# Performance work log

Hardware: AMD Instinct MI355X
Metric: run time of the kernel (lower is better)

## Reference

```python
import jax, jax.numpy as jnp
import numpy as np

B, F, T, K = 131072, 1024, 100, 32  # batch, num_features, num_trees, features per tree (sqrt(F))


def setup_inputs() -> dict:
    key = jax.random.key(0)
    kx, kw = jax.random.split(key)
    x = jax.random.normal(kx, (B, F), dtype=jnp.float32)
    # per-tree random feature selection without replacement (np.random.choice replace=False)
    rng = np.random.default_rng(0)
    idx = np.argsort(rng.random((T, F)), axis=1)[:, :K].astype(np.int32)
    feature_indices = jnp.asarray(idx)
    feature_thresholds = jnp.zeros((T, K), dtype=jnp.float32)  # lazy-init zeros in original
    feature_weights = jax.random.uniform(kw, (T, K), dtype=jnp.float32)  # torch.rand
    return {
        "x": x,
        "feature_indices": feature_indices,
        "feature_thresholds": feature_thresholds,
        "feature_weights": feature_weights,
    }


def reference(x, feature_indices, feature_thresholds, feature_weights):
    # Per tree t: ws_t = sum_k (x[:, idx[t,k]] - thr[t,k]) * w[t,k]
    # Equivalent fused form: scatter weights into a dense [T, F] matrix and do one GEMM,
    # with per-tree bias sum_k thr*w. scatter-add handles any duplicate indices identically
    # to the gather-then-sum formulation.
    T_, K_ = feature_indices.shape
    tree_ids = jnp.arange(T_, dtype=feature_indices.dtype)[:, None]  # [T,1]
    W_full = jnp.zeros((T_, x.shape[1]), dtype=x.dtype).at[tree_ids, feature_indices].add(feature_weights)
    bias = jnp.sum(feature_thresholds * feature_weights, axis=1)  # [T]
    ws = x @ W_full.T - bias[None, :]  # [B, T]
    p = jax.nn.sigmoid(ws)
    pm = jnp.mean(p, axis=1)  # mean over trees; mean(1-p) = 1 - mean(p)
    return jnp.stack([1.0 - pm, pm], axis=1)  # [B, 2]
```

## Files before the change

kernel.cpp:

```cpp
#include <hip/hip_runtime.h>
#include <math.h>

constexpr int Bn = 131072;
constexpr int Fn = 1024;
constexpr int Tn = 100;
constexpr int Kn = 32;

constexpr int TP = 112;
constexpr int NF = TP / 16;
constexpr int BK = 32;
constexpr int NT = Fn / BK;
constexpr int BM = 128;
constexpr int MW = 32;
constexpr int BLOCK = 256;
constexpr int GRID = Bn / BM;

typedef __attribute__((ext_vector_type(8))) short bf16x8;
typedef __attribute__((ext_vector_type(4))) float f32x4;

using gptr_t = const __attribute__((address_space(1))) void*;
using lptr_t = __attribute__((address_space(3))) void*;

__device__ inline unsigned short f2bf(float f) {
    uint32_t u = __float_as_uint(f);
    return (unsigned short)((u + 0x7FFFu + ((u >> 16) & 1u)) >> 16);
}

__global__ __launch_bounds__(64)
void rf_prep(const int* __restrict__ fidx, const float* __restrict__ fthr,
             const float* __restrict__ fw,
             unsigned short* __restrict__ wt, float* __restrict__ bias)
{
    const int t    = blockIdx.x;
    const int lane = threadIdx.x;

    int4 z = make_int4(0, 0, 0, 0);
    int4* rowp = (int4*)(wt + (size_t)t * Fn);
    rowp[lane * 2 + 0] = z;
    rowp[lane * 2 + 1] = z;
    __syncthreads();

    float bsum = 0.f;
    if (t < Tn && lane < Kn) {
        const int   idx = fidx[t * Kn + lane];
        const float w   = fw[t * Kn + lane];
        const float th  = fthr[t * Kn + lane];
        wt[(size_t)t * Fn + idx] = f2bf(w);
        bsum = th * w;
    }
#pragma unroll
    for (int d = 1; d < 64; d <<= 1) bsum += __shfl_xor(bsum, d, 64);
    if (lane == 0) bias[t] = (t < Tn) ? bsum : 0.f;
}

__global__ __launch_bounds__(BLOCK)
void rf_gemm(const float* __restrict__ x,
             const unsigned short* __restrict__ wt,
             const float* __restrict__ bias,
             float* __restrict__ out)
{
    __shared__ float lds[2][BM * BK];

    const int lane = threadIdx.x & 63;
    const int wid  = threadIdx.x >> 6;
    const int rb   = blockIdx.x * BM;

    const int s_row = lane >> 3;
    const int s_c16 = (lane & 7) ^ s_row;

    const int a_rl  = lane & 15;
    const int a_xor = lane & 7;
    const int a_cb  = (lane >> 4) * 2;

    f32x4 acc[2][NF];
#pragma unroll
    for (int m = 0; m < 2; ++m)
#pragma unroll
        for (int f = 0; f < NF; ++f) acc[m][f] = (f32x4){0.f, 0.f, 0.f, 0.f};

    auto stage = [&](int t, int bsel) {
#pragma unroll
        for (int i = 0; i < 4; ++i) {
            const int win = wid * 4 + i;
            const int row = win * 8 + s_row;
            const float* src = x + (size_t)(rb + row) * Fn + t * BK + s_c16 * 4;
            float* dst = &lds[bsel][win * 256];
            __builtin_amdgcn_global_load_lds((gptr_t)src, (lptr_t)dst, 16, 0, 0);
        }
    };

    stage(0, 0);
    __syncthreads();

    for (int t = 0; t < NT; ++t) {
        const int cur = t & 1;
        if (t + 1 < NT) stage(t + 1, cur ^ 1);

        bf16x8 bfr[NF];
#pragma unroll
        for (int f = 0; f < NF; ++f) {
            const unsigned short* bp =
                wt + (size_t)(f * 16 + a_rl) * Fn + t * BK + (lane >> 4) * 8;
            bfr[f] = *(const bf16x8*)bp;
        }

        const float* buf = lds[cur];
        bf16x8 af[2];
#pragma unroll
        for (int m = 0; m < 2; ++m) {
            const int row = wid * MW + m * 16 + a_rl;
            const float* rp = buf + row * BK;
            float4 lo = *(const float4*)(rp + (((a_cb + 0) ^ a_xor) * 4));
            float4 hi = *(const float4*)(rp + (((a_cb + 1) ^ a_xor) * 4));
            bf16x8 v;
            v[0] = (short)f2bf(lo.x); v[1] = (short)f2bf(lo.y);
            v[2] = (short)f2bf(lo.z); v[3] = (short)f2bf(lo.w);
            v[4] = (short)f2bf(hi.x); v[5] = (short)f2bf(hi.y);
            v[6] = (short)f2bf(hi.z); v[7] = (short)f2bf(hi.w);
            af[m] = v;
        }

#pragma unroll
        for (int m = 0; m < 2; ++m)
#pragma unroll
            for (int f = 0; f < NF; ++f)
                acc[m][f] = __builtin_amdgcn_mfma_f32_16x16x32_bf16(
                    af[m], bfr[f], acc[m][f], 0, 0, 0);

        __syncthreads();
    }

    const int col = lane & 15;
    float psum[2][4] = {};
#pragma unroll
    for (int f = 0; f < NF; ++f) {
        const int  n     = f * 16 + col;
        const bool valid = n < Tn;
        const float bv   = bias[n];
#pragma unroll
        for (int m = 0; m < 2; ++m)
#pragma unroll
            for (int r = 0; r < 4; ++r) {
                const float ws = acc[m][f][r] - bv;
                const float p  = 1.f / (1.f + __expf(-ws));
                if (valid) psum[m][r] += p;
            }
    }
#pragma unroll
    for (int m = 0; m < 2; ++m)
#pragma unroll
        for (int r = 0; r < 4; ++r)
#pragma unroll
            for (int d = 1; d < 16; d <<= 1)
                psum[m][r] += __shfl_xor(psum[m][r], d, 64);

    const int g = lane >> 4;
#pragma unroll
    for (int m = 0; m < 2; ++m) {
        if (col < 4) {
            const int r   = col;
            const int row = rb + wid * MW + m * 16 + g * 4 + r;
            const float pm = psum[m][r] * (1.0f / Tn);
            *(float2*)(out + (size_t)row * 2) = make_float2(1.0f - pm, pm);
        }
    }
}

extern "C" void kernel_launch(void* const* d_in, const int* in_sizes, int n_in,
                              void* d_out, int out_size, void* d_ws, size_t ws_size,
                              hipStream_t stream) {
    const float* x    = (const float*)d_in[0];
    const int*   fidx = (const int*)  d_in[1];
    const float* fthr = (const float*)d_in[2];
    const float* fw   = (const float*)d_in[3];
    float*       out  = (float*)d_out;

    unsigned short* wt   = (unsigned short*)d_ws;
    float*          bias = (float*)((char*)d_ws + (size_t)TP * Fn * 2);

    rf_prep<<<TP, 64, 0, stream>>>(fidx, fthr, fw, wt, bias);
    rf_gemm<<<GRID, BLOCK, 0, stream>>>(x, wt, bias, out);
}
```

Measured before the change: 168.3 us.

## Double K-tile to 64, make LDS per-wave, and software-pipeline with manual vmcnt waits

Raises the K-tile to 64 and gives each wave its own LDS slice, so the block-wide __syncthreads is replaced by per-wave s_waitcnt vmcnt/lgkmcnt counts. The loop is unrolled by two and ping-pongs register buffers for the B fragments, prefetching the next tile's weights and staging the next x tile while MFMAs run. The goal is to remove barrier stalls and hide global-load latency. The risks are correctness of the hand-tuned vmcnt counts and higher register pressure under launch_bounds(256,2).

```diff
diff --git a/kernel.cpp b/kernel.cpp
--- a/kernel.cpp
+++ b/kernel.cpp
@@ -8,7 +8,8 @@
 
 constexpr int TP = 112;
 constexpr int NF = TP / 16;
-constexpr int BK = 32;
+constexpr int BK = 64;
+constexpr int KS = BK / 32;
 constexpr int NT = Fn / BK;
 constexpr int BM = 128;
 constexpr int MW = 32;
@@ -53,7 +54,7 @@
     if (lane == 0) bias[t] = (t < Tn) ? bsum : 0.f;
 }
 
-__global__ __launch_bounds__(BLOCK)
+__global__ __launch_bounds__(BLOCK, 2)
 void rf_gemm(const float* __restrict__ x,
              const unsigned short* __restrict__ wt,
              const float* __restrict__ bias,
@@ -65,12 +66,10 @@
     const int wid  = threadIdx.x >> 6;
     const int rb   = blockIdx.x * BM;
 
-    const int s_row = lane >> 3;
-    const int s_c16 = (lane & 7) ^ s_row;
-
-    const int a_rl  = lane & 15;
-    const int a_xor = lane & 7;
-    const int a_cb  = (lane >> 4) * 2;
+    const int s_r = lane >> 4;
+    const int s_p = lane & 15;
+    const int a_L = lane & 15;
+    const int a_g = lane >> 4;
 
     f32x4 acc[2][NF];
 #pragma unroll
@@ -80,54 +79,83 @@
 
     auto stage = [&](int t, int bsel) {
 #pragma unroll
-        for (int i = 0; i < 4; ++i) {
-            const int win = wid * 4 + i;
-            const int row = win * 8 + s_row;
-            const float* src = x + (size_t)(rb + row) * Fn + t * BK + s_c16 * 4;
-            float* dst = &lds[bsel][win * 256];
+        for (int i = 0; i < 8; ++i) {
+            const int row = i * 4 + s_r;
+            const int c   = s_p ^ (row & 15);
+            const float* src = x + (size_t)(rb + wid * MW + row) * Fn + t * BK + c * 4;
+            float* dst = &lds[bsel][wid * (MW * BK) + i * 256];
             __builtin_amdgcn_global_load_lds((gptr_t)src, (lptr_t)dst, 16, 0, 0);
         }
     };
 
+    auto loadB = [&](int t, bf16x8 (&bfr)[KS][NF]) {
+#pragma unroll
+        for (int ks = 0; ks < KS; ++ks)
+#pragma unroll
+            for (int f = 0; f < NF; ++f) {
+                const unsigned short* bp =
+                    wt + (size_t)(f * 16 + a_L) * Fn + t * BK + ks * 32 + a_g * 8;
+                bfr[ks][f] = *(const bf16x8*)bp;
+            }
+    };
+
+    auto readA = [&](int bsel, bf16x8 (&af)[KS][2]) {
+        const float* buf = &lds[bsel][wid * (MW * BK)];
+#pragma unroll
+        for (int ks = 0; ks < KS; ++ks)
+#pragma unroll
+            for (int m = 0; m < 2; ++m) {
+                const float* rp = buf + (m * 16 + a_L) * BK;
+                const int c0 = ks * 8 + a_g * 2;
+                float4 lo = *(const float4*)(rp + ((c0 ^ a_L) * 4));
+                float4 hi = *(const float4*)(rp + (((c0 + 1) ^ a_L) * 4));
+                bf16x8 v;
+                v[0] = (short)f2bf(lo.x); v[1] = (short)f2bf(lo.y);
+                v[2] = (short)f2bf(lo.z); v[3] = (short)f2bf(lo.w);
+                v[4] = (short)f2bf(hi.x); v[5] = (short)f2bf(hi.y);
+                v[6] = (short)f2bf(hi.z); v[7] = (short)f2bf(hi.w);
+                af[ks][m] = v;
+            }
+    };
+
+    auto mfma_all = [&](bf16x8 (&af)[KS][2], bf16x8 (&bfr)[KS][NF]) {
+#pragma unroll
+        for (int ks = 0; ks < KS; ++ks)
+#pragma unroll
+            for (int m = 0; m < 2; ++m)
+#pragma unroll
+                for (int f = 0; f < NF; ++f)
+                    acc[m][f] = __builtin_amdgcn_mfma_f32_16x16x32_bf16(
+                        af[ks][m], bfr[ks][f], acc[m][f], 0, 0, 0);
+    };
+
+    bf16x8 bA[KS][NF], bB[KS][NF];
+    bf16x8 af[KS][2];
+
     stage(0, 0);
-    __syncthreads();
-
-    for (int t = 0; t < NT; ++t) {
-        const int cur = t & 1;
-        if (t + 1 < NT) stage(t + 1, cur ^ 1);
-
-        bf16x8 bfr[NF];
-#pragma unroll
-        for (int f = 0; f < NF; ++f) {
-            const unsigned short* bp =
-                wt + (size_t)(f * 16 + a_rl) * Fn + t * BK + (lane >> 4) * 8;
-            bfr[f] = *(const bf16x8*)bp;
+    __builtin_amdgcn_sched_barrier(0);
+    loadB(0, bA);
+    __builtin_amdgcn_sched_barrier(0);
+    stage(1, 1);
+
+    for (int t = 0; t < NT; t += 2) {
+        loadB(t + 1, bB);
+        asm volatile("s_waitcnt vmcnt(36)" ::: "memory");
+        readA(0, af);
+        asm volatile("s_waitcnt lgkmcnt(0)" ::: "memory");
+        if (t + 2 < NT) stage(t + 2, 0);
+        mfma_all(af, bA);
+
+        if (t + 2 < NT) {
+            loadB(t + 2, bA);
+            asm volatile("s_waitcnt vmcnt(36)" ::: "memory");
+        } else {
+            asm volatile("s_waitcnt vmcnt(14)" ::: "memory");
         }
-
-        const float* buf = lds[cur];
-        bf16x8 af[2];
-#pragma unroll
-        for (int m = 0; m < 2; ++m) {
-            const int row = wid * MW + m * 16 + a_rl;
-            const float* rp = buf + row * BK;
-            float4 lo = *(const float4*)(rp + (((a_cb + 0) ^ a_xor) * 4));
-            float4 hi = *(const float4*)(rp + (((a_cb + 1) ^ a_xor) * 4));
-            bf16x8 v;
-            v[0] = (short)f2bf(lo.x); v[1] = (short)f2bf(lo.y);
-            v[2] = (short)f2bf(lo.z); v[3] = (short)f2bf(lo.w);
-            v[4] = (short)f2bf(hi.x); v[5] = (short)f2bf(hi.y);
-            v[6] = (short)f2bf(hi.z); v[7] = (short)f2bf(hi.w);
-            af[m] = v;
-        }
-
-#pragma unroll
-        for (int m = 0; m < 2; ++m)
-#pragma unroll
-            for (int f = 0; f < NF; ++f)
-                acc[m][f] = __builtin_amdgcn_mfma_f32_16x16x32_bf16(
-                    af[m], bfr[f], acc[m][f], 0, 0, 0);
-
-        __syncthreads();
+        readA(1, af);
+        asm volatile("s_waitcnt lgkmcnt(0)" ::: "memory");
+        if (t + 3 < NT) stage(t + 3, 1);
+        mfma_all(af, bB);
     }
 
     const int col = lane & 15;
```

Result: faster. 159.3 us (-5.3%).

## Load A directly from global into registers with double-buffered register prefetch

Applied to the files above, without the earlier changes.

Removes the LDS staging buffer and the per-iteration block barrier. Each wave now loads its x rows straight from global memory into registers, one float4 pair per lane per k-step. Loads are double-buffered in registers with explicit s_waitcnt vmcnt counts, so the next k-step's A and B fragments are in flight while the current MFMAs run. This adds register pressure, and the global access pattern becomes strided per row, 32-byte pieces from 16 rows per wave, which may coalesce less well than the earlier LDS staging. The hand-coded vmcnt values also depend on the compiler not reordering or splitting the loads.

```diff
diff --git a/kernel.cpp b/kernel.cpp
--- a/kernel.cpp
+++ b/kernel.cpp
@@ -6,24 +6,29 @@
 constexpr int Tn = 100;
 constexpr int Kn = 32;
 
-constexpr int TP = 112;
-constexpr int NF = TP / 16;
-constexpr int BK = 32;
-constexpr int NT = Fn / BK;
-constexpr int BM = 128;
-constexpr int MW = 32;
+constexpr int TP  = 112;
+constexpr int NF  = TP / 16;
+constexpr int NKS = Fn / 32;
+constexpr int BM  = 128;
+constexpr int MW  = 32;
 constexpr int BLOCK = 256;
-constexpr int GRID = Bn / BM;
+constexpr int GRID  = Bn / BM;
 
 typedef __attribute__((ext_vector_type(8))) short bf16x8;
 typedef __attribute__((ext_vector_type(4))) float f32x4;
 
-using gptr_t = const __attribute__((address_space(1))) void*;
-using lptr_t = __attribute__((address_space(3))) void*;
-
 __device__ inline unsigned short f2bf(float f) {
     uint32_t u = __float_as_uint(f);
     return (unsigned short)((u + 0x7FFFu + ((u >> 16) & 1u)) >> 16);
+}
+
+__device__ inline bf16x8 cvt8(float4 lo, float4 hi) {
+    bf16x8 v;
+    v[0] = (short)f2bf(lo.x); v[1] = (short)f2bf(lo.y);
+    v[2] = (short)f2bf(lo.z); v[3] = (short)f2bf(lo.w);
+    v[4] = (short)f2bf(hi.x); v[5] = (short)f2bf(hi.y);
+    v[6] = (short)f2bf(hi.z); v[7] = (short)f2bf(hi.w);
+    return v;
 }
 
 __global__ __launch_bounds__(64)
@@ -53,82 +58,93 @@
     if (lane == 0) bias[t] = (t < Tn) ? bsum : 0.f;
 }
 
+#define ISSUE(ks, A0, A1, A2, A3, B0, B1, B2, B3, B4, B5, B6) do {        \
+    A0 = *(const float4*)(pa0 + (ks) * 32);                               \
+    A1 = *(const float4*)(pa0 + (ks) * 32 + 4);                          \
+    A2 = *(const float4*)(pa1 + (ks) * 32);                              \
+    A3 = *(const float4*)(pa1 + (ks) * 32 + 4);                          \
+    B0 = *(const bf16x8*)(pb0 + (ks) * 32);                              \
+    B1 = *(const bf16x8*)(pb1 + (ks) * 32);                              \
+    B2 = *(const bf16x8*)(pb2 + (ks) * 32);                              \
+    B3 = *(const bf16x8*)(pb3 + (ks) * 32);                              \
+    B4 = *(const bf16x8*)(pb4 + (ks) * 32);                              \
+    B5 = *(const bf16x8*)(pb5 + (ks) * 32);                              \
+    B6 = *(const bf16x8*)(pb6 + (ks) * 32);                              \
+} while (0)
+
+#define STEP(A0, A1, A2, A3, B0, B1, B2, B3, B4, B5, B6) do {             \
+    bf16x8 fa0 = cvt8(A0, A1);                                            \
+    bf16x8 fa1 = cvt8(A2, A3);                                            \
+    acc00 = __builtin_amdgcn_mfma_f32_16x16x32_bf16(fa0, B0, acc00,0,0,0);\
+    acc01 = __builtin_amdgcn_mfma_f32_16x16x32_bf16(fa0, B1, acc01,0,0,0);\
+    acc02 = __builtin_amdgcn_mfma_f32_16x16x32_bf16(fa0, B2, acc02,0,0,0);\
+    acc03 = __builtin_amdgcn_mfma_f32_16x16x32_bf16(fa0, B3, acc03,0,0,0);\
+    acc04 = __builtin_amdgcn_mfma_f32_16x16x32_bf16(fa0, B4, acc04,0,0,0);\
+    acc05 = __builtin_amdgcn_mfma_f32_16x16x32_bf16(fa0, B5, acc05,0,0,0);\
+    acc06 = __builtin_amdgcn_mfma_f32_16x16x32_bf16(fa0, B6, acc06,0,0,0);\
+    acc10 = __builtin_amdgcn_mfma_f32_16x16x32_bf16(fa1, B0, acc10,0,0,0);\
+    acc11 = __builtin_amdgcn_mfma_f32_16x16x32_bf16(fa1, B1, acc11,0,0,0);\
+    acc12 = __builtin_amdgcn_mfma_f32_16x16x32_bf16(fa1, B2, acc12,0,0,0);\
+    acc13 = __builtin_amdgcn_mfma_f32_16x16x32_bf16(fa1, B3, acc13,0,0,0);\
+    acc14 = __builtin_amdgcn_mfma_f32_16x16x32_bf16(fa1, B4, acc14,0,0,0);\
+    acc15 = __builtin_amdgcn_mfma_f32_16x16x32_bf16(fa1, B5, acc15,0,0,0);\
+    acc16 = __builtin_amdgcn_mfma_f32_16x16x32_bf16(fa1, B6, acc16,0,0,0);\
+} while (0)
+
 __global__ __launch_bounds__(BLOCK)
 void rf_gemm(const float* __restrict__ x,
              const unsigned short* __restrict__ wt,
              const float* __restrict__ bias,
              float* __restrict__ out)
 {
-    __shared__ float lds[2][BM * BK];
-
     const int lane = threadIdx.x & 63;
     const int wid  = threadIdx.x >> 6;
     const int rb   = blockIdx.x * BM;
+    const int r    = lane & 15;
+    const int g    = lane >> 4;
 
-    const int s_row = lane >> 3;
-    const int s_c16 = (lane & 7) ^ s_row;
+    const float* pa0 = x + (size_t)(rb + wid * MW + r) * Fn + g * 8;
+    const float* pa1 = pa0 + (size_t)16 * Fn;
+    const unsigned short* pb0 = wt + (size_t)(0 * 16 + r) * Fn + g * 8;
+    const unsigned short* pb1 = wt + (size_t)(1 * 16 + r) * Fn + g * 8;
+    const unsigned short* pb2 = wt + (size_t)(2 * 16 + r) * Fn + g * 8;
+    const unsigned short* pb3 = wt + (size_t)(3 * 16 + r) * Fn + g * 8;
+    const unsigned short* pb4 = wt + (size_t)(4 * 16 + r) * Fn + g * 8;
+    const unsigned short* pb5 = wt + (size_t)(5 * 16 + r) * Fn + g * 8;
+    const unsigned short* pb6 = wt + (size_t)(6 * 16 + r) * Fn + g * 8;
 
-    const int a_rl  = lane & 15;
-    const int a_xor = lane & 7;
-    const int a_cb  = (lane >> 4) * 2;
+    f32x4 acc00 = {0,0,0,0}, acc01 = {0,0,0,0}, acc02 = {0,0,0,0},
+          acc03 = {0,0,0,0}, acc04 = {0,0,0,0}, acc05 = {0,0,0,0},
+          acc06 = {0,0,0,0};
+    f32x4 acc10 = {0,0,0,0}, acc11 = {0,0,0,0}, acc12 = {0,0,0,0},
+          acc13 = {0,0,0,0}, acc14 = {0,0,0,0}, acc15 = {0,0,0,0},
+          acc16 = {0,0,0,0};
 
-    f32x4 acc[2][NF];
-#pragma unroll
-    for (int m = 0; m < 2; ++m)
-#pragma unroll
-        for (int f = 0; f < NF; ++f) acc[m][f] = (f32x4){0.f, 0.f, 0.f, 0.f};
+    float4 cA0, cA1, cA2, cA3, nA0, nA1, nA2, nA3;
+    bf16x8 cB0, cB1, cB2, cB3, cB4, cB5, cB6;
+    bf16x8 nB0, nB1, nB2, nB3, nB4, nB5, nB6;
 
-    auto stage = [&](int t, int bsel) {
-#pragma unroll
-        for (int i = 0; i < 4; ++i) {
-            const int win = wid * 4 + i;
-            const int row = win * 8 + s_row;
-            const float* src = x + (size_t)(rb + row) * Fn + t * BK + s_c16 * 4;
-            float* dst = &lds[bsel][win * 256];
-            __builtin_amdgcn_global_load_lds((gptr_t)src, (lptr_t)dst, 16, 0, 0);
-        }
-    };
-
-    stage(0, 0);
-    __syncthreads();
-
-    for (int t = 0; t < NT; ++t) {
-        const int cur = t & 1;
-        if (t + 1 < NT) stage(t + 1, cur ^ 1);
-
-        bf16x8 bfr[NF];
-#pragma unroll
-        for (int f = 0; f < NF; ++f) {
-            const unsigned short* bp =
-                wt + (size_t)(f * 16 + a_rl) * Fn + t * BK + (lane >> 4) * 8;
-            bfr[f] = *(const bf16x8*)bp;
-        }
-
-        const float* buf = lds[cur];
-        bf16x8 af[2];
-#pragma unroll
-        for (int m = 0; m < 2; ++m) {
-            const int row = wid * MW + m * 16 + a_rl;
-            const float* rp = buf + row * BK;
-            float4 lo = *(const float4*)(rp + (((a_cb + 0) ^ a_xor) * 4));
-            float4 hi = *(const float4*)(rp + (((a_cb + 1) ^ a_xor) * 4));
-            bf16x8 v;
-            v[0] = (short)f2bf(lo.x); v[1] = (short)f2bf(lo.y);
-            v[2] = (short)f2bf(lo.z); v[3] = (short)f2bf(lo.w);
-            v[4] = (short)f2bf(hi.x); v[5] = (short)f2bf(hi.y);
-            v[6] = (short)f2bf(hi.z); v[7] = (short)f2bf(hi.w);
-            af[m] = v;
-        }
+    ISSUE(0, cA0, cA1, cA2, cA3, cB0, cB1, cB2, cB3, cB4, cB5, cB6);
 
 #pragma unroll
-        for (int m = 0; m < 2; ++m)
-#pragma unroll
-            for (int f = 0; f < NF; ++f)
-                acc[m][f] = __builtin_amdgcn_mfma_f32_16x16x32_bf16(
-                    af[m], bfr[f], acc[m][f], 0, 0, 0);
+    for (int ks = 0; ks < NKS; ks += 2) {
+        ISSUE(ks + 1, nA0, nA1, nA2, nA3, nB0, nB1, nB2, nB3, nB4, nB5, nB6);
+        asm volatile("s_waitcnt vmcnt(11)" ::: "memory");
+        STEP(cA0, cA1, cA2, cA3, cB0, cB1, cB2, cB3, cB4, cB5, cB6);
 
-        __syncthreads();
+        if (ks + 2 < NKS) {
+            ISSUE(ks + 2, cA0, cA1, cA2, cA3, cB0, cB1, cB2, cB3, cB4, cB5, cB6);
+            asm volatile("s_waitcnt vmcnt(11)" ::: "memory");
+        } else {
+            asm volatile("s_waitcnt vmcnt(0)" ::: "memory");
+        }
+        STEP(nA0, nA1, nA2, nA3, nB0, nB1, nB2, nB3, nB4, nB5, nB6);
     }
+
+    f32x4 accA[2][NF] = {
+        { acc00, acc01, acc02, acc03, acc04, acc05, acc06 },
+        { acc10, acc11, acc12, acc13, acc14, acc15, acc16 }
+    };
 
     const int col = lane & 15;
     float psum[2][4] = {};
@@ -140,27 +156,26 @@
 #pragma unroll
         for (int m = 0; m < 2; ++m)
 #pragma unroll
-            for (int r = 0; r < 4; ++r) {
-                const float ws = acc[m][f][r] - bv;
+            for (int q = 0; q < 4; ++q) {
+                const float ws = accA[m][f][q] - bv;
                 const float p  = 1.f / (1.f + __expf(-ws));
-                if (valid) psum[m][r] += p;
+                if (valid) psum[m][q] += p;
             }
     }
 #pragma unroll
     for (int m = 0; m < 2; ++m)
 #pragma unroll
-        for (int r = 0; r < 4; ++r)
+        for (int q = 0; q < 4; ++q)
 #pragma unroll
             for (int d = 1; d < 16; d <<= 1)
-                psum[m][r] += __shfl_xor(psum[m][r], d, 64);
+                psum[m][q] += __shfl_xor(psum[m][q], d, 64);
 
-    const int g = lane >> 4;
 #pragma unroll
     for (int m = 0; m < 2; ++m) {
         if (col < 4) {
-            const int r   = col;
-            const int row = rb + wid * MW + m * 16 + g * 4 + r;
-            const float pm = psum[m][r] * (1.0f / Tn);
+            const int q   = col;
+            const int row = rb + wid * MW + m * 16 + g * 4 + q;
+            const float pm = psum[m][q] * (1.0f / Tn);
             *(float2*)(out + (size_t)row * 2) = make_float2(1.0f - pm, pm);
         }
     }
```

New measurement: 264.0 us. 1.57x slower.
